# Kernel tuning notes

Hardware: AMD Instinct MI355X
Metric: run time of the kernel (lower is better)

## Reference

```python
import jax, jax.numpy as jnp
import numpy as np

B, S, D = 16, 1024, 512
H, DH = 8, 64  # heads, dim_head


def setup_inputs() -> dict:
    key = jax.random.key(0)
    ks = jax.random.split(key, 7)
    x = jax.random.normal(ks[0], (B, S, D), dtype=jnp.float32)
    # variable sequence lengths in [1, S]
    seq_lens = jnp.maximum(jax.random.randint(ks[1], (B,), 0, S + 1), 1).astype(jnp.int32)
    w_std = 0.02
    Wq = jax.random.normal(ks[2], (D, D), dtype=jnp.float32) * w_std
    Wk = jax.random.normal(ks[3], (D, D), dtype=jnp.float32) * w_std
    Wv = jax.random.normal(ks[4], (D, D), dtype=jnp.float32) * w_std
    Wo = jax.random.normal(ks[5], (D, D), dtype=jnp.float32) * w_std
    bo = jnp.zeros((D,), dtype=jnp.float32)
    return {"x": x, "seq_lens": seq_lens, "Wq": Wq, "Wk": Wk, "Wv": Wv, "Wo": Wo, "bo": bo}


def reference(x, seq_lens, Wq, Wk, Wv, Wo, bo):
    # x: [B, S, D] padded ragged batch; seq_lens: [B] valid token counts.
    # Equivalent to the per-batch SDPA loop over jagged sequences: attention
    # is computed only among the valid tokens of each sequence.
    scale = DH ** -0.5
    q = (x @ Wq).reshape(B, S, H, DH)
    k = (x @ Wk).reshape(B, S, H, DH)
    v = (x @ Wv).reshape(B, S, H, DH)
    scores = jnp.einsum('bqhd,bkhd->bhqk', q, k) * scale  # [B,H,S,S]
    valid = jnp.arange(S)[None, :] < seq_lens[:, None]     # [B,S] token mask
    neg_inf = jnp.finfo(scores.dtype).min
    scores = jnp.where(valid[:, None, None, :], scores, neg_inf)
    attn = jax.nn.softmax(scores, axis=-1)
    out = jnp.einsum('bhqk,bkhd->bqhd', attn, v).reshape(B, S, D)
    out = out @ Wo + bo  # to_out Linear (dropout=0 / eval)
    return out * valid[:, :, None]  # zero padded query positions
```

## Files before the change

kernel.cpp:

```cpp
#include <hip/hip_runtime.h>
#include <hip/hip_bf16.h>

typedef __bf16 bf16_t;
typedef __attribute__((ext_vector_type(4))) __bf16 bf16x4;
typedef __attribute__((ext_vector_type(8))) __bf16 bf16x8;
typedef __attribute__((ext_vector_type(4))) float f32x4;

#define MFMA16(a, b, c) __builtin_amdgcn_mfma_f32_16x16x32_bf16((a), (b), (c), 0, 0, 0)

#define BB 16
#define SS 1024
#define DD 512
#define HH 8
#define DH 64
#define NTOK (BB * SS)
#define QSCALE 0.18033688f

typedef const __attribute__((address_space(1))) void gas_void;
typedef __attribute__((address_space(3))) void las_void;

__device__ __forceinline__ void async_cp16(const void* g, void* l) {
    __builtin_amdgcn_global_load_lds((gas_void*)g, (las_void*)l, 16, 0, 0);
}

__device__ __forceinline__ bf16x8 frag_ld(const char* sm, int row, int kk, int g) {
    int r7 = row & 7;
    int base = row * 128 + ((g & 1) << 3);
    int c0 = ((kk << 2) + (g >> 1)) ^ r7;
    int c1 = ((kk << 2) + 2 + (g >> 1)) ^ r7;
    bf16x4 lo = *(const bf16x4*)(sm + base + (c0 << 4));
    bf16x4 hi = *(const bf16x4*)(sm + base + (c1 << 4));
    return __builtin_shufflevector(lo, hi, 0, 1, 2, 3, 4, 5, 6, 7);
}

__device__ __forceinline__ bf16x8 frag_at(const char* smrow, int a0, int a1) {
    bf16x4 lo = *(const bf16x4*)(smrow + a0);
    bf16x4 hi = *(const bf16x4*)(smrow + a1);
    return __builtin_shufflevector(lo, hi, 0, 1, 2, 3, 4, 5, 6, 7);
}

__global__ __launch_bounds__(256) void cast_x_k(const float* __restrict__ x,
                                                bf16_t* __restrict__ xb, int n4) {
    int i = blockIdx.x * 256 + threadIdx.x;
    if (i < n4) {
        float4 v = ((const float4*)x)[i];
        bf16x4 o;
        o[0] = (bf16_t)v.x; o[1] = (bf16_t)v.y; o[2] = (bf16_t)v.z; o[3] = (bf16_t)v.w;
        *(bf16x4*)(xb + (size_t)i * 4) = o;
    }
}

__global__ __launch_bounds__(256) void transpose_w_k(const float* __restrict__ W0,
                                                     const float* __restrict__ W1,
                                                     const float* __restrict__ W2,
                                                     const float* __restrict__ W3,
                                                     bf16_t* __restrict__ Wt) {
    __shared__ float t[32][33];
    int z = blockIdx.z;
    const float* W = (z == 0) ? W0 : (z == 1) ? W1 : (z == 2) ? W2 : W3;
    bf16_t* out = Wt + (size_t)z * DD * DD;
    int n0 = blockIdx.x * 32, k0 = blockIdx.y * 32;
    int tx = threadIdx.x, ty = threadIdx.y;
#pragma unroll
    for (int i = 0; i < 32; i += 8)
        t[ty + i][tx] = W[(size_t)(k0 + ty + i) * DD + n0 + tx];
    __syncthreads();
#pragma unroll
    for (int i = 0; i < 32; i += 8)
        out[(size_t)(n0 + ty + i) * DD + k0 + tx] = (bf16_t)t[tx][ty + i];
}

__global__ void build_q_k(const int* __restrict__ sl, ushort* __restrict__ items,
                          int* __restrict__ meta) {
    int l = threadIdx.x;
    __shared__ int s_b[BB], s_cnt[BB], s_start[BB];
    if (l < BB) {
        int len = sl[l];
        int rank = 0;
        for (int j = 0; j < BB; ++j) {
            int lj = sl[j];
            if (lj > len || (lj == len && j < l)) ++rank;
        }
        s_b[rank] = l;
        s_cnt[rank] = ((len + 127) >> 7) * HH;
    }
    __syncthreads();
    if (l < BB) {
        int st = 0;
        for (int j = 0; j < l; ++j) st += s_cnt[j];
        s_start[l] = st;
        if (l == BB - 1) { meta[0] = st + s_cnt[l]; meta[1] = 0; }
    }
    __syncthreads();
    if (l < BB) {
        int b = s_b[l], st = s_start[l], c = s_cnt[l];
        int nqt = c >> 3;
        for (int i = 0; i < c; ++i) {
            int h = i / nqt, qt = i - h * nqt;
            items[st + i] = (ushort)((((b << 3) | h) << 3) | qt);
        }
    }
}

template <int MODE>
__global__ __launch_bounds__(256) void gemm_k(const bf16_t* __restrict__ A,
                                              const bf16_t* __restrict__ WtBase,
                                              bf16_t* __restrict__ oQ,
                                              bf16_t* __restrict__ oK,
                                              bf16_t* __restrict__ oVt,
                                              float* __restrict__ oO,
                                              const float* __restrict__ bo,
                                              const int* __restrict__ seq_lens) {
    __shared__ __align__(16) char smem[32768];
    char* smA = smem;
    char* smB = smem + 16384;
    const int tid = threadIdx.x;
    const int l = tid & 63, w = tid >> 6;
    const int lr = l & 15, g = l >> 4;
    const int bm = blockIdx.x, bn = blockIdx.y;
    const int z = (MODE == 0) ? blockIdx.z : 3;
    const bf16_t* Wt = WtBase + (size_t)z * DD * DD;
    const int row0 = bm * 128;
    const int col0 = bn * 128;
    const int wm = (w >> 1) * 64, wn = (w & 1) * 64;

    f32x4 acc[4][4] = {};

    for (int kt = 0; kt < 8; ++kt) {
        const int k0 = kt * 64;
        __syncthreads();
#pragma unroll
        for (int it = 0; it < 4; ++it) {
            int cl = it * 256 + tid;
            int m = cl >> 3, p = cl & 7, c = p ^ (m & 7);
            async_cp16(A + (size_t)(row0 + m) * DD + k0 + c * 8, smA + cl * 16);
        }
#pragma unroll
        for (int it = 0; it < 4; ++it) {
            int cl = it * 256 + tid;
            int m = cl >> 3, p = cl & 7, c = p ^ (m & 7);
            async_cp16(Wt + (size_t)(col0 + m) * DD + k0 + c * 8, smB + cl * 16);
        }
        __syncthreads();
#pragma unroll
        for (int kk = 0; kk < 2; ++kk) {
            bf16x8 af[4], bfr[4];
#pragma unroll
            for (int i = 0; i < 4; ++i) af[i] = frag_ld(smA, wm + i * 16 + lr, kk, g);
#pragma unroll
            for (int j = 0; j < 4; ++j) bfr[j] = frag_ld(smB, wn + j * 16 + lr, kk, g);
#pragma unroll
            for (int i = 0; i < 4; ++i)
#pragma unroll
                for (int j = 0; j < 4; ++j)
                    acc[i][j] = MFMA16(af[i], bfr[j], acc[i][j]);
        }
    }

    if (MODE == 0) {
        if (z < 2) {
            bf16_t* outp = (z == 0) ? oQ : oK;
            const float sc = (z == 0) ? QSCALE : 1.f;
#pragma unroll
            for (int i = 0; i < 4; ++i) {
                int mrow = row0 + wm + i * 16 + g * 4;
#pragma unroll
                for (int j = 0; j < 4; ++j) {
                    int n = col0 + wn + j * 16 + lr;
                    int h = n >> 6, dh = n & 63;
#pragma unroll
                    for (int r = 0; r < 4; ++r) {
                        int m = mrow + r;
                        int b = m >> 10, s = m & 1023;
                        outp[((size_t)((b * HH + h) * SS + s)) * DH + dh] =
                            (bf16_t)(acc[i][j][r] * sc);
                    }
                }
            }
        } else {
            __syncthreads();
            bf16_t* tsm = (bf16_t*)smem;
#pragma unroll
            for (int i = 0; i < 4; ++i)
#pragma unroll
                for (int j = 0; j < 4; ++j)
#pragma unroll
                    for (int r = 0; r < 4; ++r)
                        tsm[(wm + i * 16 + g * 4 + r) * 128 + wn + j * 16 + lr] =
                            (bf16_t)acc[i][j][r];
            __syncthreads();
            int nloc = tid >> 1;
            int mbase = (tid & 1) * 64;
            int n = col0 + nloc;
            int h = n >> 6, dh = n & 63;
            int b = row0 >> 10;
            int s0 = (row0 & 1023) + mbase;
            bf16_t* dst = oVt + ((size_t)((b * HH + h) * DH + dh)) * SS + s0;
#pragma unroll
            for (int mm = 0; mm < 64; mm += 8) {
                bf16x8 v;
#pragma unroll
                for (int e = 0; e < 8; ++e) v[e] = tsm[(mbase + mm + e) * 128 + nloc];
                *(bf16x8*)(dst + mm) = v;
            }
        }
    } else {
        int b = row0 >> 10;
        int len = seq_lens[b];
#pragma unroll
        for (int i = 0; i < 4; ++i) {
            int mrow = row0 + wm + i * 16 + g * 4;
#pragma unroll
            for (int j = 0; j < 4; ++j) {
                int n = col0 + wn + j * 16 + lr;
                float bias = bo[n];
#pragma unroll
                for (int r = 0; r < 4; ++r) {
                    int m = mrow + r;
                    int s = m & 1023;
                    oO[(size_t)m * DD + n] = (s < len) ? (acc[i][j][r] + bias) : 0.f;
                }
            }
        }
    }
}

__global__ __launch_bounds__(256) void attn_k(const bf16_t* __restrict__ Q,
                                              const bf16_t* __restrict__ K,
                                              const bf16_t* __restrict__ Vt,
                                              bf16_t* __restrict__ O,
                                              const int* __restrict__ seq_lens,
                                              const ushort* __restrict__ items,
                                              int* __restrict__ meta) {
    __shared__ __align__(16) char smem[49152];
    __shared__ int s_item;
    const int tid = threadIdx.x, l = tid & 63, w = tid >> 6;
    const int lr = l & 15, g = l >> 4;
    const int nitems = meta[0];
    int* cursor = meta + 1;

    const int x0 = lr * 128 + ((g & 1) << 3);
    const int xr = lr & 7;
    const int a00 = x0 + ((((g >> 1) + 0) ^ xr) << 4);
    const int a01 = x0 + ((((g >> 1) + 2) ^ xr) << 4);
    const int a10 = x0 + ((((g >> 1) + 4) ^ xr) << 4);
    const int a11 = x0 + ((((g >> 1) + 6) ^ xr) << 4);

    for (;;) {
        if (tid == 0) s_item = atomicAdd(cursor, 1);
        __syncthreads();
        const int ii = s_item;
        if (ii >= nitems) return;
        const int itv = items[ii];
        const int qt = itv & 7, bh = itv >> 3;
        const int b = bh >> 3;
        const int len = seq_lens[b];
        const int q0 = qt * 128;
        const int h = bh & 7;

        const bf16_t* kbase = K + (size_t)bh * SS * DH;
        const bf16_t* vbase = Vt + (size_t)bh * DH * SS;

        bf16x8 bq[2][2];
#pragma unroll
        for (int qs = 0; qs < 2; ++qs) {
            const bf16_t* qp = Q + ((size_t)bh * SS + q0 + w * 32 + qs * 16 + lr) * DH;
#pragma unroll
            for (int kk = 0; kk < 2; ++kk) {
                bf16x4 lo = *(const bf16x4*)(qp + kk * 32 + 4 * g);
                bf16x4 hi = *(const bf16x4*)(qp + kk * 32 + 16 + 4 * g);
                bq[qs][kk] = __builtin_shufflevector(lo, hi, 0, 1, 2, 3, 4, 5, 6, 7);
            }
        }

        f32x4 oacc[2][4] = {};
        float mrun[2] = {-1e30f, -1e30f};
        float lpart[2] = {0.f, 0.f};

        const int nkt = (len + 63) >> 6;

        auto stage = [&](int buf, int key0) {
            char* smK = smem + buf * 16384;
            char* smV = smK + 8192;
#pragma unroll
            for (int it = 0; it < 2; ++it) {
                int cl = it * 256 + tid;
                int m = cl >> 3, p = cl & 7, c = p ^ (m & 7);
                async_cp16(kbase + (size_t)(key0 + m) * DH + c * 8, smK + cl * 16);
            }
#pragma unroll
            for (int it = 0; it < 2; ++it) {
                int cl = it * 256 + tid;
                int m = cl >> 3, p = cl & 7, c = p ^ (m & 7);
                async_cp16(vbase + (size_t)m * SS + key0 + c * 8, smV + cl * 16);
            }
        };

        stage(0, 0);
        if (nkt > 1) stage(1, 64);
        int cur = 0;

        for (int kt = 0; kt < nkt; ++kt) {
            const int key0 = kt * 64;
            if (kt + 1 < nkt) {
                asm volatile("s_waitcnt vmcnt(4)" ::: "memory");
            } else {
                asm volatile("s_waitcnt vmcnt(0)" ::: "memory");
            }
            __builtin_amdgcn_s_barrier();
            __builtin_amdgcn_sched_barrier(0);
            if (kt + 2 < nkt) {
                int b2 = (cur >= 1) ? cur - 1 : 2;
                stage(b2, key0 + 128);
            }
            const char* smK = smem + cur * 16384;
            const char* smV = smK + 8192;

            f32x4 pacc[2][4] = {};
#pragma unroll
            for (int nt = 0; nt < 4; ++nt) {
                bf16x8 ak0 = frag_at(smK + nt * 2048, a00, a01);
                bf16x8 ak1 = frag_at(smK + nt * 2048, a10, a11);
#pragma unroll
                for (int qs = 0; qs < 2; ++qs) {
                    pacc[qs][nt] = MFMA16(ak0, bq[qs][0], pacc[qs][nt]);
                    pacc[qs][nt] = MFMA16(ak1, bq[qs][1], pacc[qs][nt]);
                }
            }

            const bool full = (key0 + 64 <= len);

#pragma unroll
            for (int qs = 0; qs < 2; ++qs) {
                float mloc = -1e30f;
                if (full) {
#pragma unroll
                    for (int nt = 0; nt < 4; ++nt)
#pragma unroll
                        for (int r = 0; r < 4; ++r) mloc = fmaxf(mloc, pacc[qs][nt][r]);
                } else {
#pragma unroll
                    for (int nt = 0; nt < 4; ++nt)
#pragma unroll
                        for (int r = 0; r < 4; ++r) {
                            int kg = key0 + nt * 16 + 4 * g + r;
                            float s = (kg < len) ? pacc[qs][nt][r] : -1e30f;
                            pacc[qs][nt][r] = s;
                            mloc = fmaxf(mloc, s);
                        }
                }
                mloc = fmaxf(mloc, __shfl_xor(mloc, 16, 64));
                mloc = fmaxf(mloc, __shfl_xor(mloc, 32, 64));

                float mn;
                if (__all(mloc <= mrun[qs])) {
                    mn = mrun[qs];
                } else {
                    mn = fmaxf(mrun[qs], mloc);
                    float corr = __builtin_amdgcn_exp2f(mrun[qs] - mn);
                    mrun[qs] = mn;
                    lpart[qs] *= corr;
                    float cb[4];
#pragma unroll
                    for (int r = 0; r < 4; ++r) cb[r] = __shfl(corr, 4 * g + r, 64);
#pragma unroll
                    for (int dt = 0; dt < 4; ++dt)
#pragma unroll
                        for (int r = 0; r < 4; ++r) oacc[qs][dt][r] *= cb[r];
                }

                float ls = 0.f;
#pragma unroll
                for (int nt = 0; nt < 4; ++nt)
#pragma unroll
                    for (int r = 0; r < 4; ++r) {
                        float p = __builtin_amdgcn_exp2f(pacc[qs][nt][r] - mn);
                        pacc[qs][nt][r] = p;
                        ls += p;
                    }
                lpart[qs] += ls;

                bf16x8 pa[2];
#pragma unroll
                for (int kf = 0; kf < 2; ++kf)
#pragma unroll
                    for (int j = 0; j < 8; ++j)
                        pa[kf][j] = (bf16_t)pacc[qs][2 * kf + (j >> 2)][j & 3];
#pragma unroll
                for (int kf = 0; kf < 2; ++kf)
#pragma unroll
                    for (int dt = 0; dt < 4; ++dt) {
                        bf16x8 bv = frag_at(smV + dt * 2048, kf ? a10 : a00,
                                            kf ? a11 : a01);
                        oacc[qs][dt] = MFMA16(pa[kf], bv, oacc[qs][dt]);
                    }
            }
            cur = (cur == 2) ? 0 : cur + 1;
        }

#pragma unroll
        for (int qs = 0; qs < 2; ++qs) {
            float lt = lpart[qs];
            lt += __shfl_xor(lt, 16, 64);
            lt += __shfl_xor(lt, 32, 64);
#pragma unroll
            for (int r = 0; r < 4; ++r) {
                float inv = 1.f / __shfl(lt, 4 * g + r, 64);
                int q = q0 + w * 32 + qs * 16 + 4 * g + r;
                size_t orow = ((size_t)b * SS + q) * DD;
#pragma unroll
                for (int dt = 0; dt < 4; ++dt)
                    O[orow + h * DH + dt * 16 + lr] = (bf16_t)(oacc[qs][dt][r] * inv);
            }
        }
    }
}

extern "C" void kernel_launch(void* const* d_in, const int* in_sizes, int n_in,
                              void* d_out, int out_size, void* d_ws, size_t ws_size,
                              hipStream_t stream) {
    const float* x = (const float*)d_in[0];
    const int* seq_lens = (const int*)d_in[1];
    const float* Wq = (const float*)d_in[2];
    const float* Wk = (const float*)d_in[3];
    const float* Wv = (const float*)d_in[4];
    const float* Wo = (const float*)d_in[5];
    const float* bo = (const float*)d_in[6];
    float* out = (float*)d_out;

    char* ws = (char*)d_ws;
    const size_t SEG = (size_t)NTOK * DD * sizeof(bf16_t);
    bf16_t* xb = (bf16_t*)ws;
    bf16_t* qb = (bf16_t*)(ws + SEG);
    bf16_t* kb = (bf16_t*)(ws + 2 * SEG);
    bf16_t* vtb = (bf16_t*)(ws + 3 * SEG);
    bf16_t* wt = (bf16_t*)(ws + 4 * SEG);
    ushort* items = (ushort*)(ws + 4 * SEG + (size_t)4 * DD * DD * sizeof(bf16_t));
    int* meta = (int*)(items + 1024);
    bf16_t* ab = xb;

    build_q_k<<<dim3(1), dim3(64), 0, stream>>>(seq_lens, items, meta);
    cast_x_k<<<dim3((NTOK * DD / 4) / 256), dim3(256), 0, stream>>>(x, xb, NTOK * DD / 4);
    transpose_w_k<<<dim3(16, 16, 4), dim3(32, 8), 0, stream>>>(Wq, Wk, Wv, Wo, wt);
    gemm_k<0><<<dim3(NTOK / 128, DD / 128, 3), dim3(256), 0, stream>>>(
        xb, wt, qb, kb, vtb, nullptr, nullptr, nullptr);
    attn_k<<<dim3(768), dim3(256), 0, stream>>>(qb, kb, vtb, ab, seq_lens, items, meta);
    gemm_k<2><<<dim3(NTOK / 128, DD / 128, 1), dim3(256), 0, stream>>>(
        ab, wt, nullptr, nullptr, nullptr, out, bo, seq_lens);
}
```

Baseline: 136.2 us.

## Store Q/K/V in MFMA-fragment-native layout for contiguous attention loads

The QKV projection epilogue now stages results through swizzled shared memory and writes Q, K and V^T in a pre-tiled fragment order. Each lane's MFMA operand becomes one contiguous 16-byte chunk, so the attention kernel can read Q with a single vector load per fragment, async-copy K/V tiles linearly without swizzle arithmetic, and read LDS fragments as one bf16x8 instead of two bf16x4 loads. V fragments are also hoisted into registers once per key tile. The cost is a more complex projection epilogue, an extra LDS round-trip and barrier for Q/K, and higher register pressure in attention.

```diff
diff --git a/kernel.cpp b/kernel.cpp
--- a/kernel.cpp
+++ b/kernel.cpp
@@ -33,10 +33,8 @@
     return __builtin_shufflevector(lo, hi, 0, 1, 2, 3, 4, 5, 6, 7);
 }
 
-__device__ __forceinline__ bf16x8 frag_at(const char* smrow, int a0, int a1) {
-    bf16x4 lo = *(const bf16x4*)(smrow + a0);
-    bf16x4 hi = *(const bf16x4*)(smrow + a1);
-    return __builtin_shufflevector(lo, hi, 0, 1, 2, 3, 4, 5, 6, 7);
+__device__ __forceinline__ bf16x8 fragl(const char* sm, int idx, int l) {
+    return *(const bf16x8*)(sm + (idx * 64 + l) * 16);
 }
 
 __global__ __launch_bounds__(256) void cast_x_k(const float* __restrict__ x,
@@ -158,50 +156,61 @@
     }
 
     if (MODE == 0) {
+        __syncthreads();
+        char* tl = smem;
+        const float sc = (z == 0) ? QSCALE : 1.f;
+#pragma unroll
+        for (int i = 0; i < 4; ++i)
+#pragma unroll
+            for (int j = 0; j < 4; ++j)
+#pragma unroll
+                for (int r = 0; r < 4; ++r) {
+                    int s = wm + i * 16 + g * 4 + r;
+                    int n = wn + j * 16 + lr;
+                    int nb = 2 * n;
+                    int byte = s * 256 + ((((nb >> 4) ^ (s & 7)) << 4) | (nb & 15));
+                    *(bf16_t*)(tl + byte) = (bf16_t)(acc[i][j][r] * sc);
+                }
+        __syncthreads();
+        const int b = row0 >> 10, s0 = row0 & 1023;
         if (z < 2) {
-            bf16_t* outp = (z == 0) ? oQ : oK;
-            const float sc = (z == 0) ? QSCALE : 1.f;
-#pragma unroll
-            for (int i = 0; i < 4; ++i) {
-                int mrow = row0 + wm + i * 16 + g * 4;
-#pragma unroll
-                for (int j = 0; j < 4; ++j) {
-                    int n = col0 + wn + j * 16 + lr;
-                    int h = n >> 6, dh = n & 63;
-#pragma unroll
-                    for (int r = 0; r < 4; ++r) {
-                        int m = mrow + r;
-                        int b = m >> 10, s = m & 1023;
-                        outp[((size_t)((b * HH + h) * SS + s)) * DH + dh] =
-                            (bf16_t)(acc[i][j][r] * sc);
-                    }
-                }
+            bf16_t* dst = (z == 0) ? oQ : oK;
+#pragma unroll
+            for (int c8 = 0; c8 < 8; ++c8) {
+                int combo = c8 * 4 + w;
+                int kk = combo & 1, t = (combo >> 1) & 7, hl = combo >> 4;
+                int s = 16 * t + lr;
+                bf16x4 pr[2];
+#pragma unroll
+                for (int jj = 0; jj < 2; ++jj) {
+                    int nb = 128 * hl + 64 * kk + 32 * jj + 8 * g;
+                    int byte = s * 256 + ((((nb >> 4) ^ (s & 7)) << 4) | (nb & 15));
+                    pr[jj] = *(const bf16x4*)(tl + byte);
+                }
+                bf16x8 v = __builtin_shufflevector(pr[0], pr[1], 0, 1, 2, 3, 4, 5, 6, 7);
+                int bhh = b * 8 + (col0 >> 6) + hl;
+                int tg = (s0 >> 4) + t;
+                *(bf16x8*)(dst + (((size_t)bhh * 64 + tg) * 2 + kk) * 512 + l * 8) = v;
             }
         } else {
-            __syncthreads();
-            bf16_t* tsm = (bf16_t*)smem;
-#pragma unroll
-            for (int i = 0; i < 4; ++i)
-#pragma unroll
-                for (int j = 0; j < 4; ++j)
-#pragma unroll
-                    for (int r = 0; r < 4; ++r)
-                        tsm[(wm + i * 16 + g * 4 + r) * 128 + wn + j * 16 + lr] =
-                            (bf16_t)acc[i][j][r];
-            __syncthreads();
-            int nloc = tid >> 1;
-            int mbase = (tid & 1) * 64;
-            int n = col0 + nloc;
-            int h = n >> 6, dh = n & 63;
-            int b = row0 >> 10;
-            int s0 = (row0 & 1023) + mbase;
-            bf16_t* dst = oVt + ((size_t)((b * HH + h) * DH + dh)) * SS + s0;
-#pragma unroll
-            for (int mm = 0; mm < 64; mm += 8) {
+#pragma unroll
+            for (int c8 = 0; c8 < 8; ++c8) {
+                int combo = c8 * 4 + w;
+                int kk = combo & 1, dt = (combo >> 1) & 3;
+                int st = (combo >> 3) & 1, hl = (combo >> 4) & 1;
                 bf16x8 v;
 #pragma unroll
-                for (int e = 0; e < 8; ++e) v[e] = tsm[(mbase + mm + e) * 128 + nloc];
-                *(bf16x8*)(dst + mm) = v;
+                for (int j = 0; j < 8; ++j) {
+                    int s = 64 * st + 32 * kk + 16 * (j >> 2) + 4 * g + (j & 3);
+                    int n = 64 * hl + 16 * dt + lr;
+                    int nb = 2 * n;
+                    int byte = s * 256 + ((((nb >> 4) ^ (s & 7)) << 4) | (nb & 15));
+                    v[j] = *(const bf16_t*)(tl + byte);
+                }
+                int bhh = b * 8 + (col0 >> 6) + hl;
+                int stg = (s0 >> 6) + st;
+                *(bf16x8*)(oVt + ((((size_t)bhh * 16 + stg) * 4 + dt) * 2 + kk) * 512 +
+                           l * 8) = v;
             }
         }
     } else {
@@ -225,9 +234,9 @@
     }
 }
 
-__global__ __launch_bounds__(256) void attn_k(const bf16_t* __restrict__ Q,
-                                              const bf16_t* __restrict__ K,
-                                              const bf16_t* __restrict__ Vt,
+__global__ __launch_bounds__(256) void attn_k(const bf16_t* __restrict__ Qf,
+                                              const bf16_t* __restrict__ Kf,
+                                              const bf16_t* __restrict__ Vf,
                                               bf16_t* __restrict__ O,
                                               const int* __restrict__ seq_lens,
                                               const ushort* __restrict__ items,
@@ -238,13 +247,6 @@
     const int lr = l & 15, g = l >> 4;
     const int nitems = meta[0];
     int* cursor = meta + 1;
-
-    const int x0 = lr * 128 + ((g & 1) << 3);
-    const int xr = lr & 7;
-    const int a00 = x0 + ((((g >> 1) + 0) ^ xr) << 4);
-    const int a01 = x0 + ((((g >> 1) + 2) ^ xr) << 4);
-    const int a10 = x0 + ((((g >> 1) + 4) ^ xr) << 4);
-    const int a11 = x0 + ((((g >> 1) + 6) ^ xr) << 4);
 
     for (;;) {
         if (tid == 0) s_item = atomicAdd(cursor, 1);
@@ -258,19 +260,17 @@
         const int q0 = qt * 128;
         const int h = bh & 7;
 
-        const bf16_t* kbase = K + (size_t)bh * SS * DH;
-        const bf16_t* vbase = Vt + (size_t)bh * DH * SS;
+        const bf16_t* kfb = Kf + (size_t)bh * 65536;
+        const bf16_t* vfb = Vf + (size_t)bh * 65536;
 
         bf16x8 bq[2][2];
 #pragma unroll
         for (int qs = 0; qs < 2; ++qs) {
-            const bf16_t* qp = Q + ((size_t)bh * SS + q0 + w * 32 + qs * 16 + lr) * DH;
-#pragma unroll
-            for (int kk = 0; kk < 2; ++kk) {
-                bf16x4 lo = *(const bf16x4*)(qp + kk * 32 + 4 * g);
-                bf16x4 hi = *(const bf16x4*)(qp + kk * 32 + 16 + 4 * g);
-                bq[qs][kk] = __builtin_shufflevector(lo, hi, 0, 1, 2, 3, 4, 5, 6, 7);
-            }
+            int t = (q0 >> 4) + 2 * w + qs;
+#pragma unroll
+            for (int kk = 0; kk < 2; ++kk)
+                bq[qs][kk] = *(const bf16x8*)(
+                    Qf + (((size_t)bh * 64 + t) * 2 + kk) * 512 + l * 8);
         }
 
         f32x4 oacc[2][4] = {};
@@ -279,25 +279,25 @@
 
         const int nkt = (len + 63) >> 6;
 
-        auto stage = [&](int buf, int key0) {
+        auto stage = [&](int buf, int kti) {
             char* smK = smem + buf * 16384;
             char* smV = smK + 8192;
+            const bf16_t* ks = kfb + kti * 4096;
+            const bf16_t* vs = vfb + kti * 4096;
 #pragma unroll
             for (int it = 0; it < 2; ++it) {
                 int cl = it * 256 + tid;
-                int m = cl >> 3, p = cl & 7, c = p ^ (m & 7);
-                async_cp16(kbase + (size_t)(key0 + m) * DH + c * 8, smK + cl * 16);
+                async_cp16(ks + cl * 8, smK + cl * 16);
             }
 #pragma unroll
             for (int it = 0; it < 2; ++it) {
                 int cl = it * 256 + tid;
-                int m = cl >> 3, p = cl & 7, c = p ^ (m & 7);
-                async_cp16(vbase + (size_t)m * SS + key0 + c * 8, smV + cl * 16);
+                async_cp16(vs + cl * 8, smV + cl * 16);
             }
         };
 
         stage(0, 0);
-        if (nkt > 1) stage(1, 64);
+        if (nkt > 1) stage(1, 1);
         int cur = 0;
 
         for (int kt = 0; kt < nkt; ++kt) {
@@ -311,16 +311,23 @@
             __builtin_amdgcn_sched_barrier(0);
             if (kt + 2 < nkt) {
                 int b2 = (cur >= 1) ? cur - 1 : 2;
-                stage(b2, key0 + 128);
+                stage(b2, kt + 2);
             }
             const char* smK = smem + cur * 16384;
             const char* smV = smK + 8192;
 
+            bf16x8 bv[4][2];
+#pragma unroll
+            for (int dt = 0; dt < 4; ++dt)
+#pragma unroll
+                for (int kk = 0; kk < 2; ++kk)
+                    bv[dt][kk] = fragl(smV, dt * 2 + kk, l);
+
             f32x4 pacc[2][4] = {};
 #pragma unroll
             for (int nt = 0; nt < 4; ++nt) {
-                bf16x8 ak0 = frag_at(smK + nt * 2048, a00, a01);
-                bf16x8 ak1 = frag_at(smK + nt * 2048, a10, a11);
+                bf16x8 ak0 = fragl(smK, nt * 2 + 0, l);
+                bf16x8 ak1 = fragl(smK, nt * 2 + 1, l);
 #pragma unroll
                 for (int qs = 0; qs < 2; ++qs) {
                     pacc[qs][nt] = MFMA16(ak0, bq[qs][0], pacc[qs][nt]);
@@ -389,11 +396,8 @@
 #pragma unroll
                 for (int kf = 0; kf < 2; ++kf)
 #pragma unroll
-                    for (int dt = 0; dt < 4; ++dt) {
-                        bf16x8 bv = frag_at(smV + dt * 2048, kf ? a10 : a00,
-                                            kf ? a11 : a01);
-                        oacc[qs][dt] = MFMA16(pa[kf], bv, oacc[qs][dt]);
-                    }
+                    for (int dt = 0; dt < 4; ++dt)
+                        oacc[qs][dt] = MFMA16(pa[kf], bv[dt][kf], oacc[qs][dt]);
             }
             cur = (cur == 2) ? 0 : cur + 1;
         }
```

Result: faster. 122.6 us (-10.0%).
